# Kernel tuning notes

Hardware: AMD Instinct MI355X
Metric: run time of the kernel (lower is better)

The kernel has to match this reference:

```python
import jax, jax.numpy as jnp
import numpy as np

N = 50000
E = 600000
D = 128  # hidden_dim


def setup_inputs() -> dict:
    key = jax.random.key(0)
    k_x, k_ei, k_ea, k_w1, k_b1, k_w2, k_b2 = jax.random.split(key, 7)
    x = jax.random.normal(k_x, (N, D), dtype=jnp.float32)
    edge_index = jax.random.randint(k_ei, (2, E), 0, N, dtype=jnp.int64)
    edge_attr = jax.random.normal(k_ea, (E, D), dtype=jnp.float32)
    # torch nn.Linear init scale ~ 1/sqrt(fan_in); stored as [in, out] here
    s1 = 1.0 / np.sqrt(2 * D)
    s2 = 1.0 / np.sqrt(D)
    W1 = jax.random.uniform(k_w1, (2 * D, D), dtype=jnp.float32, minval=-s1, maxval=s1)
    b1 = jax.random.uniform(k_b1, (D,), dtype=jnp.float32, minval=-s1, maxval=s1)
    W2 = jax.random.uniform(k_w2, (D, D), dtype=jnp.float32, minval=-s2, maxval=s2)
    b2 = jax.random.uniform(k_b2, (D,), dtype=jnp.float32, minval=-s2, maxval=s2)
    return {"x": x, "edge_index": edge_index, "edge_attr": edge_attr,
            "W1": W1, "b1": b1, "W2": W2, "b2": b2}


def reference(x, edge_index, edge_attr, W1, b1, W2, b2):
    row, col = edge_index[0], edge_index[1]
    # scatter-add edge features to both endpoints (index_add_ twice)
    edge_aggr = jnp.zeros((x.shape[0], edge_attr.shape[1]), dtype=x.dtype)
    edge_aggr = edge_aggr.at[row].add(edge_attr).at[col].add(edge_attr)
    node_features = jnp.concatenate([x, edge_aggr], axis=1)  # [N, 2D]
    h = jax.nn.relu(node_features @ W1 + b1)
    return h @ W2 + b2
```

## Files before the change

### kernel.cpp

```cpp
#include <hip/hip_runtime.h>

#define D 128

__global__ __launch_bounds__(256) void degree_kernel(
    const int* __restrict__ ei, int* __restrict__ deg, int twoE) {
  int i = blockIdx.x * blockDim.x + threadIdx.x;
  if (i < twoE) atomicAdd(&deg[ei[i]], 1);
}

__global__ __launch_bounds__(1024) void scan_kernel(
    const int* __restrict__ deg, int* __restrict__ off,
    int* __restrict__ cursor, int n) {
  __shared__ int sdata[1024];
  __shared__ int carry_s;
  int tid = threadIdx.x;
  if (tid == 0) carry_s = 0;
  __syncthreads();
  for (int base = 0; base < n; base += 1024) {
    int i = base + tid;
    int v = (i < n) ? deg[i] : 0;
    sdata[tid] = v;
    __syncthreads();
#pragma unroll
    for (int s = 1; s < 1024; s <<= 1) {
      int t = (tid >= s) ? sdata[tid - s] : 0;
      __syncthreads();
      sdata[tid] += t;
      __syncthreads();
    }
    int carry = carry_s;
    if (i < n) {
      int excl = carry + sdata[tid] - v;
      off[i] = excl;
      cursor[i] = excl;
    }
    __syncthreads();
    if (tid == 0) carry_s = carry + sdata[1023];
    __syncthreads();
  }
}

__global__ __launch_bounds__(256) void fill_kernel(
    const int* __restrict__ ei, int* __restrict__ cursor,
    int* __restrict__ elist, int E, int twoE) {
  int i = blockIdx.x * blockDim.x + threadIdx.x;
  if (i >= twoE) return;
  int node = ei[i];
  int e = (i < E) ? i : i - E;
  int pos = atomicAdd(&cursor[node], 1);
  elist[pos] = e;
}

__global__ __launch_bounds__(128) void gather_kernel(
    const float* __restrict__ edge_attr, const int* __restrict__ off,
    const int* __restrict__ deg, const int* __restrict__ elist,
    float* __restrict__ aggr, int N) {
  int node = blockIdx.x;
  int j = threadIdx.x;
  int s = off[node];
  int d = deg[node];
  float acc = 0.f;
  int k = 0;
  for (; k + 4 <= d; k += 4) {
    int e0 = elist[s + k + 0];
    int e1 = elist[s + k + 1];
    int e2 = elist[s + k + 2];
    int e3 = elist[s + k + 3];
    float v0 = edge_attr[(long long)e0 * D + j];
    float v1 = edge_attr[(long long)e1 * D + j];
    float v2 = edge_attr[(long long)e2 * D + j];
    float v3 = edge_attr[(long long)e3 * D + j];
    acc += (v0 + v1) + (v2 + v3);
  }
  for (; k < d; ++k) {
    int e = elist[s + k];
    acc += edge_attr[(long long)e * D + j];
  }
  aggr[(long long)node * D + j] = acc;
}

template <int K, bool RELU>
__global__ __launch_bounds__(256) void mlp_layer(
    const float* __restrict__ A0,
    const float* __restrict__ A1,
    const float* __restrict__ W,
    const float* __restrict__ bias,
    float* __restrict__ outp, int N) {
  constexpr int KC = 64;
  __shared__ float As[64][KC];
  __shared__ float Ws[KC][D];
  const int t = threadIdx.x;
  const int tx = t & 31;
  const int ty = t >> 5;
  const int row0 = blockIdx.x * 64;
  const int col = tx * 4;

  float acc[8][4];
  {
    float4 b = reinterpret_cast<const float4*>(bias)[tx];
#pragma unroll
    for (int i = 0; i < 8; ++i) {
      acc[i][0] = b.x; acc[i][1] = b.y; acc[i][2] = b.z; acc[i][3] = b.w;
    }
  }

  for (int kc = 0; kc < K; kc += KC) {
#pragma unroll
    for (int p = 0; p < 4; ++p) {
      int r = p * 16 + (t >> 4);
      int c4 = (t & 15);
      int gk = kc + c4 * 4;
      int gr = row0 + r;
      float4 v = make_float4(0.f, 0.f, 0.f, 0.f);
      if (gr < N) {
        const float* src;
        if (K == 256) {
          src = (gk < 128) ? (A0 + (long long)gr * 128 + gk)
                           : (A1 + (long long)gr * 128 + (gk - 128));
        } else {
          src = A0 + (long long)gr * 128 + gk;
        }
        v = *reinterpret_cast<const float4*>(src);
      }
      *reinterpret_cast<float4*>(&As[r][c4 * 4]) = v;
    }
#pragma unroll
    for (int p = 0; p < 8; ++p) {
      int r = p * 8 + (t >> 5);
      int c4 = (t & 31);
      float4 v = *reinterpret_cast<const float4*>(W + (long long)(kc + r) * D + c4 * 4);
      *reinterpret_cast<float4*>(&Ws[r][c4 * 4]) = v;
    }
    __syncthreads();

#pragma unroll
    for (int k4 = 0; k4 < KC / 4; ++k4) {
      float4 wv[4];
#pragma unroll
      for (int kk = 0; kk < 4; ++kk)
        wv[kk] = *reinterpret_cast<const float4*>(&Ws[k4 * 4 + kk][col]);
#pragma unroll
      for (int i = 0; i < 8; ++i) {
        float4 av = *reinterpret_cast<const float4*>(&As[ty * 8 + i][k4 * 4]);
        acc[i][0] += av.x * wv[0].x + av.y * wv[1].x + av.z * wv[2].x + av.w * wv[3].x;
        acc[i][1] += av.x * wv[0].y + av.y * wv[1].y + av.z * wv[2].y + av.w * wv[3].y;
        acc[i][2] += av.x * wv[0].z + av.y * wv[1].z + av.z * wv[2].z + av.w * wv[3].z;
        acc[i][3] += av.x * wv[0].w + av.y * wv[1].w + av.z * wv[2].w + av.w * wv[3].w;
      }
    }
    __syncthreads();
  }

#pragma unroll
  for (int i = 0; i < 8; ++i) {
    int gr = row0 + ty * 8 + i;
    if (gr < N) {
      float4 o = make_float4(acc[i][0], acc[i][1], acc[i][2], acc[i][3]);
      if (RELU) {
        o.x = fmaxf(o.x, 0.f); o.y = fmaxf(o.y, 0.f);
        o.z = fmaxf(o.z, 0.f); o.w = fmaxf(o.w, 0.f);
      }
      reinterpret_cast<float4*>(outp + (long long)gr * D)[tx] = o;
    }
  }
}

extern "C" void kernel_launch(void* const* d_in, const int* in_sizes, int n_in,
                              void* d_out, int out_size, void* d_ws, size_t ws_size,
                              hipStream_t stream) {
  const float* x         = (const float*)d_in[0];
  const int*   ei        = (const int*)d_in[1];
  const float* edge_attr = (const float*)d_in[2];
  const float* W1        = (const float*)d_in[3];
  const float* b1        = (const float*)d_in[4];
  const float* W2        = (const float*)d_in[5];
  const float* b2        = (const float*)d_in[6];
  const int N = in_sizes[0] / D;
  const int E = in_sizes[2] / D;
  const int twoE = 2 * E;

  float* aggr = (float*)d_ws;
  float* h    = aggr + (size_t)N * D;
  int* deg    = (int*)h;
  int* off    = deg + N;
  int* cursor = off + N;
  int* elist  = cursor + N;

  hipMemsetAsync(deg, 0, (size_t)N * sizeof(int), stream);

  degree_kernel<<<(twoE + 255) / 256, 256, 0, stream>>>(ei, deg, twoE);
  scan_kernel<<<1, 1024, 0, stream>>>(deg, off, cursor, N);
  fill_kernel<<<(twoE + 255) / 256, 256, 0, stream>>>(ei, cursor, elist, E, twoE);
  gather_kernel<<<N, 128, 0, stream>>>(edge_attr, off, deg, elist, aggr, N);

  int gb = (N + 63) / 64;
  mlp_layer<256, true ><<<gb, 256, 0, stream>>>(x, aggr, W1, b1, h, N);
  mlp_layer<128, false><<<gb, 256, 0, stream>>>(h, nullptr, W2, b2, (float*)d_out, N);
}
```

Before: 900.0 us.

## Parallelize degree scan, vectorize degree count, and fuse both MLP layers

Replaces the single-block serial prefix scan over node degrees with a three-kernel multi-block scan (block sums, partial scan, final scan). The degree count now loads four indices per thread as an int4. The two MLP layers are fused into one kernel that keeps the hidden activations in shared memory, so the intermediate h no longer goes to global memory and back. The fused kernel uses more shared memory per block (weights tile plus a 64x128 activation tile), which may lower occupancy.

```diff
diff --git a/kernel.cpp b/kernel.cpp
--- a/kernel.cpp
+++ b/kernel.cpp
@@ -5,38 +5,77 @@
 __global__ __launch_bounds__(256) void degree_kernel(
     const int* __restrict__ ei, int* __restrict__ deg, int twoE) {
   int i = blockIdx.x * blockDim.x + threadIdx.x;
-  if (i < twoE) atomicAdd(&deg[ei[i]], 1);
-}
-
-__global__ __launch_bounds__(1024) void scan_kernel(
-    const int* __restrict__ deg, int* __restrict__ off,
-    int* __restrict__ cursor, int n) {
-  __shared__ int sdata[1024];
-  __shared__ int carry_s;
-  int tid = threadIdx.x;
-  if (tid == 0) carry_s = 0;
+  int base = i * 4;
+  if (base + 3 < twoE) {
+    int4 v = *reinterpret_cast<const int4*>(ei + base);
+    atomicAdd(&deg[v.x], 1); atomicAdd(&deg[v.y], 1);
+    atomicAdd(&deg[v.z], 1); atomicAdd(&deg[v.w], 1);
+  } else {
+    for (int j = base; j < twoE; ++j) atomicAdd(&deg[ei[j]], 1);
+  }
+}
+
+__global__ __launch_bounds__(256) void scan_blocksum(
+    const int* __restrict__ deg, int* __restrict__ partials, int n) {
+  __shared__ int red[256];
+  int t = threadIdx.x;
+  int base = blockIdx.x * 1024 + t * 4;
+  int s = 0;
+#pragma unroll
+  for (int j = 0; j < 4; ++j) {
+    int i = base + j;
+    s += (i < n) ? deg[i] : 0;
+  }
+  red[t] = s;
   __syncthreads();
-  for (int base = 0; base < n; base += 1024) {
-    int i = base + tid;
-    int v = (i < n) ? deg[i] : 0;
-    sdata[tid] = v;
-    __syncthreads();
-#pragma unroll
-    for (int s = 1; s < 1024; s <<= 1) {
-      int t = (tid >= s) ? sdata[tid - s] : 0;
-      __syncthreads();
-      sdata[tid] += t;
-      __syncthreads();
-    }
-    int carry = carry_s;
-    if (i < n) {
-      int excl = carry + sdata[tid] - v;
-      off[i] = excl;
-      cursor[i] = excl;
-    }
-    __syncthreads();
-    if (tid == 0) carry_s = carry + sdata[1023];
-    __syncthreads();
+#pragma unroll
+  for (int w = 128; w > 0; w >>= 1) {
+    if (t < w) red[t] += red[t + w];
+    __syncthreads();
+  }
+  if (t == 0) partials[blockIdx.x] = red[0];
+}
+
+__global__ __launch_bounds__(64) void scan_partials(int* partials, int nb) {
+  __shared__ int tmp[64];
+  int t = threadIdx.x;
+  int v = (t < nb) ? partials[t] : 0;
+  tmp[t] = v;
+  __syncthreads();
+#pragma unroll
+  for (int s = 1; s < 64; s <<= 1) {
+    int a = (t >= s) ? tmp[t - s] : 0;
+    __syncthreads();
+    tmp[t] += a;
+    __syncthreads();
+  }
+  if (t < nb) partials[t] = tmp[t] - v;
+}
+
+__global__ __launch_bounds__(256) void scan_final(
+    const int* __restrict__ deg, const int* __restrict__ partials,
+    int* __restrict__ off, int* __restrict__ cursor, int n) {
+  __shared__ int red[256];
+  int t = threadIdx.x;
+  int base = blockIdx.x * 1024 + t * 4;
+  int v[4];
+#pragma unroll
+  for (int j = 0; j < 4; ++j) v[j] = (base + j < n) ? deg[base + j] : 0;
+  int tsum = v[0] + v[1] + v[2] + v[3];
+  red[t] = tsum;
+  __syncthreads();
+#pragma unroll
+  for (int s = 1; s < 256; s <<= 1) {
+    int a = (t >= s) ? red[t - s] : 0;
+    __syncthreads();
+    red[t] += a;
+    __syncthreads();
+  }
+  int e = red[t] - tsum + partials[blockIdx.x];
+#pragma unroll
+  for (int j = 0; j < 4; ++j) {
+    if (base + j < n) { off[base + j] = e; cursor[base + j] = e; }
+    e += v[j];
   }
 }
 
@@ -79,16 +118,14 @@
   aggr[(long long)node * D + j] = acc;
 }
 
-template <int K, bool RELU>
-__global__ __launch_bounds__(256) void mlp_layer(
-    const float* __restrict__ A0,
-    const float* __restrict__ A1,
-    const float* __restrict__ W,
-    const float* __restrict__ bias,
+__global__ __launch_bounds__(256) void fused_mlp(
+    const float* __restrict__ x, const float* __restrict__ aggr,
+    const float* __restrict__ W1, const float* __restrict__ b1,
+    const float* __restrict__ W2, const float* __restrict__ b2,
     float* __restrict__ outp, int N) {
   constexpr int KC = 64;
-  __shared__ float As[64][KC];
   __shared__ float Ws[KC][D];
+  __shared__ float AsHs[64 * D];
   const int t = threadIdx.x;
   const int tx = t & 31;
   const int ty = t >> 5;
@@ -97,14 +134,14 @@
 
   float acc[8][4];
   {
-    float4 b = reinterpret_cast<const float4*>(bias)[tx];
+    float4 b = reinterpret_cast<const float4*>(b1)[tx];
 #pragma unroll
     for (int i = 0; i < 8; ++i) {
       acc[i][0] = b.x; acc[i][1] = b.y; acc[i][2] = b.z; acc[i][3] = b.w;
     }
   }
 
-  for (int kc = 0; kc < K; kc += KC) {
+  for (int kc = 0; kc < 256; kc += KC) {
 #pragma unroll
     for (int p = 0; p < 4; ++p) {
       int r = p * 16 + (t >> 4);
@@ -113,26 +150,19 @@
       int gr = row0 + r;
       float4 v = make_float4(0.f, 0.f, 0.f, 0.f);
       if (gr < N) {
-        const float* src;
-        if (K == 256) {
-          src = (gk < 128) ? (A0 + (long long)gr * 128 + gk)
-                           : (A1 + (long long)gr * 128 + (gk - 128));
-        } else {
-          src = A0 + (long long)gr * 128 + gk;
-        }
+        const float* src = (gk < 128) ? (x + (long long)gr * 128 + gk)
+                                      : (aggr + (long long)gr * 128 + (gk - 128));
         v = *reinterpret_cast<const float4*>(src);
       }
-      *reinterpret_cast<float4*>(&As[r][c4 * 4]) = v;
+      *reinterpret_cast<float4*>(&AsHs[r * KC + c4 * 4]) = v;
     }
 #pragma unroll
     for (int p = 0; p < 8; ++p) {
       int r = p * 8 + (t >> 5);
-      int c4 = (t & 31);
-      float4 v = *reinterpret_cast<const float4*>(W + (long long)(kc + r) * D + c4 * 4);
-      *reinterpret_cast<float4*>(&Ws[r][c4 * 4]) = v;
-    }
-    __syncthreads();
-
+      float4 v = *reinterpret_cast<const float4*>(W1 + (long long)(kc + r) * D + (t & 31) * 4);
+      *reinterpret_cast<float4*>(&Ws[r][(t & 31) * 4]) = v;
+    }
+    __syncthreads();
 #pragma unroll
     for (int k4 = 0; k4 < KC / 4; ++k4) {
       float4 wv[4];
@@ -141,7 +171,7 @@
         wv[kk] = *reinterpret_cast<const float4*>(&Ws[k4 * 4 + kk][col]);
 #pragma unroll
       for (int i = 0; i < 8; ++i) {
-        float4 av = *reinterpret_cast<const float4*>(&As[ty * 8 + i][k4 * 4]);
+        float4 av = *reinterpret_cast<const float4*>(&AsHs[(ty * 8 + i) * KC + k4 * 4]);
         acc[i][0] += av.x * wv[0].x + av.y * wv[1].x + av.z * wv[2].x + av.w * wv[3].x;
         acc[i][1] += av.x * wv[0].y + av.y * wv[1].y + av.z * wv[2].y + av.w * wv[3].y;
         acc[i][2] += av.x * wv[0].z + av.y * wv[1].z + av.z * wv[2].z + av.w * wv[3].z;
@@ -153,13 +183,49 @@
 
 #pragma unroll
   for (int i = 0; i < 8; ++i) {
+    float4 o = make_float4(fmaxf(acc[i][0], 0.f), fmaxf(acc[i][1], 0.f),
+                           fmaxf(acc[i][2], 0.f), fmaxf(acc[i][3], 0.f));
+    *reinterpret_cast<float4*>(&AsHs[(ty * 8 + i) * D + col]) = o;
+  }
+
+  {
+    float4 b = reinterpret_cast<const float4*>(b2)[tx];
+#pragma unroll
+    for (int i = 0; i < 8; ++i) {
+      acc[i][0] = b.x; acc[i][1] = b.y; acc[i][2] = b.z; acc[i][3] = b.w;
+    }
+  }
+  for (int kc = 0; kc < 128; kc += KC) {
+#pragma unroll
+    for (int p = 0; p < 8; ++p) {
+      int r = p * 8 + (t >> 5);
+      float4 v = *reinterpret_cast<const float4*>(W2 + (long long)(kc + r) * D + (t & 31) * 4);
+      *reinterpret_cast<float4*>(&Ws[r][(t & 31) * 4]) = v;
+    }
+    __syncthreads();
+#pragma unroll
+    for (int k4 = 0; k4 < KC / 4; ++k4) {
+      float4 wv[4];
+#pragma unroll
+      for (int kk = 0; kk < 4; ++kk)
+        wv[kk] = *reinterpret_cast<const float4*>(&Ws[k4 * 4 + kk][col]);
+#pragma unroll
+      for (int i = 0; i < 8; ++i) {
+        float4 av = *reinterpret_cast<const float4*>(&AsHs[(ty * 8 + i) * D + kc + k4 * 4]);
+        acc[i][0] += av.x * wv[0].x + av.y * wv[1].x + av.z * wv[2].x + av.w * wv[3].x;
+        acc[i][1] += av.x * wv[0].y + av.y * wv[1].y + av.z * wv[2].y + av.w * wv[3].y;
+        acc[i][2] += av.x * wv[0].z + av.y * wv[1].z + av.z * wv[2].z + av.w * wv[3].z;
+        acc[i][3] += av.x * wv[0].w + av.y * wv[1].w + av.z * wv[2].w + av.w * wv[3].w;
+      }
+    }
+    __syncthreads();
+  }
+
+#pragma unroll
+  for (int i = 0; i < 8; ++i) {
     int gr = row0 + ty * 8 + i;
     if (gr < N) {
       float4 o = make_float4(acc[i][0], acc[i][1], acc[i][2], acc[i][3]);
-      if (RELU) {
-        o.x = fmaxf(o.x, 0.f); o.y = fmaxf(o.y, 0.f);
-        o.z = fmaxf(o.z, 0.f); o.w = fmaxf(o.w, 0.f);
-      }
       reinterpret_cast<float4*>(outp + (long long)gr * D)[tx] = o;
     }
   }
@@ -179,21 +245,24 @@
   const int E = in_sizes[2] / D;
   const int twoE = 2 * E;
 
-  float* aggr = (float*)d_ws;
-  float* h    = aggr + (size_t)N * D;
-  int* deg    = (int*)h;
-  int* off    = deg + N;
-  int* cursor = off + N;
-  int* elist  = cursor + N;
+  float* aggr   = (float*)d_ws;
+  int* deg      = (int*)(aggr + (size_t)N * D);
+  int* off      = deg + N;
+  int* cursor   = off + N;
+  int* partials = cursor + N;
+  int* elist    = partials + 64;
+
+  const int nb = (N + 1023) / 1024;
 
   hipMemsetAsync(deg, 0, (size_t)N * sizeof(int), stream);
 
-  degree_kernel<<<(twoE + 255) / 256, 256, 0, stream>>>(ei, deg, twoE);
-  scan_kernel<<<1, 1024, 0, stream>>>(deg, off, cursor, N);
+  degree_kernel<<<(twoE / 4 + 255) / 256, 256, 0, stream>>>(ei, deg, twoE);
+  scan_blocksum<<<nb, 256, 0, stream>>>(deg, partials, N);
+  scan_partials<<<1, 64, 0, stream>>>(partials, nb);
+  scan_final<<<nb, 256, 0, stream>>>(deg, partials, off, cursor, N);
   fill_kernel<<<(twoE + 255) / 256, 256, 0, stream>>>(ei, cursor, elist, E, twoE);
   gather_kernel<<<N, 128, 0, stream>>>(edge_attr, off, deg, elist, aggr, N);
 
   int gb = (N + 63) / 64;
-  mlp_layer<256, true ><<<gb, 256, 0, stream>>>(x, aggr, W1, b1, h, N);
-  mlp_layer<128, false><<<gb, 256, 0, stream>>>(h, nullptr, W2, b2, (float*)d_out, N);
-}
+  fused_mlp<<<gb, 256, 0, stream>>>(x, aggr, W1, b1, W2, b2, (float*)d_out, N);
+}
```

After: 819.1 us. 1.1x faster.
